# Kernel optimization log

Measured on AMD Instinct MI355X. Metric: run time of the kernel, lower is better.

Reference implementation:

```python
import jax, jax.numpy as jnp
import numpy as np

N, G, E = 100000, 32768, 1000000
F, H = 64, 64


def _mlp(x, w1, b1, w2, b2):
    # Linear -> SiLU -> Linear (matches nn.Sequential in the torch module)
    return jax.nn.silu(x @ w1 + b1) @ w2 + b2


def setup_inputs() -> dict:
    key = jax.random.key(0)
    ks = jax.random.split(key, 24)

    def lin(k, fan_in, fan_out):
        s = 1.0 / np.sqrt(fan_in)
        kw, kb = jax.random.split(k)
        w = jax.random.uniform(kw, (fan_in, fan_out), jnp.float32, -s, s)
        b = jax.random.uniform(kb, (fan_out,), jnp.float32, -s, s)
        return w, b

    node_w1, node_b1 = lin(ks[0], F, H)
    node_w2, node_b2 = lin(ks[1], H, H)
    edge_w1, edge_b1 = lin(ks[2], 6, H)
    edge_w2, edge_b2 = lin(ks[3], H, H)
    msg_w1, msg_b1 = lin(ks[4], 2 * H, H)
    msg_w2, msg_b2 = lin(ks[5], H, H)
    upd_w1, upd_b1 = lin(ks[6], H, H)
    upd_w2, upd_b2 = lin(ks[7], H, H)

    return {
        "node_features": jax.random.normal(ks[8], (N, F), jnp.float32),
        "node_pos": jax.random.normal(ks[9], (N, 3), jnp.float32),
        "grid_pos": jax.random.normal(ks[10], (G, 3), jnp.float32),
        "orientations": jax.random.normal(ks[11], (N, 3, 3), jnp.float32),
        "edge_index": jnp.stack([
            jax.random.randint(ks[12], (E,), 0, N),
            jax.random.randint(ks[13], (E,), 0, G),
        ]),
        "node_w1": node_w1, "node_b1": node_b1, "node_w2": node_w2, "node_b2": node_b2,
        "edge_w1": edge_w1, "edge_b1": edge_b1, "edge_w2": edge_w2, "edge_b2": edge_b2,
        "msg_w1": msg_w1, "msg_b1": msg_b1, "msg_w2": msg_w2, "msg_b2": msg_b2,
        "upd_w1": upd_w1, "upd_b1": upd_b1, "upd_w2": upd_w2, "upd_b2": upd_b2,
    }


def reference(node_features, node_pos, grid_pos, orientations, edge_index,
              node_w1, node_b1, node_w2, node_b2,
              edge_w1, edge_b1, edge_w2, edge_b2,
              msg_w1, msg_b1, msg_w2, msg_b2,
              upd_w1, upd_b1, upd_w2, upd_b2):
    source, target = edge_index[0], edge_index[1]
    num_grid = grid_pos.shape[0]

    # node MLP
    h_node = _mlp(node_features, node_w1, node_b1, node_w2, node_b2)  # [N,H]

    # per-edge message with orientation-aware projection
    pos_s = node_pos[source]                 # [E,3]
    rel = grid_pos[target] - pos_s           # [E,3]
    # bmm(rel[:,None,:], R[source]).squeeze(1) == einsum ei,eij->ej
    trel = jnp.einsum("ei,eij->ej", rel, orientations[source])
    edge_attr = jnp.concatenate([pos_s, trel], axis=-1)        # [E,6]
    e_feat = _mlp(edge_attr, edge_w1, edge_b1, edge_w2, edge_b2)
    msg_in = jnp.concatenate([h_node[source], e_feat], axis=-1)  # [E,2H]
    messages = _mlp(msg_in, msg_w1, msg_b1, msg_w2, msg_b2)      # [E,H]

    # scatter-mean into grid buckets (mask out-of-range targets)
    valid = (target >= 0) & (target < num_grid)
    idx = jnp.where(valid, target, 0)
    msg_masked = jnp.where(valid[:, None], messages, 0.0)
    sums = jax.ops.segment_sum(msg_masked, idx, num_segments=num_grid)
    cnts = jax.ops.segment_sum(valid.astype(jnp.float32), idx, num_segments=num_grid)
    grid_feat = sums / jnp.maximum(cnts, 1.0)[:, None]

    return _mlp(grid_feat, upd_w1, upd_b1, upd_w2, upd_b2)  # [G,H]
```

## Files before the change

### kernel.cpp

```cpp
#include <hip/hip_runtime.h>
#include <hip/hip_bf16.h>
#include <cstdint>

typedef __attribute__((ext_vector_type(8))) short short8;
typedef __attribute__((ext_vector_type(4))) float f32x4;
typedef unsigned short u16;

__device__ __forceinline__ float b2f(u16 u) {
  union { unsigned int i; float f; } v; v.i = ((unsigned int)u) << 16; return v.f;
}
__device__ __forceinline__ u16 f2b(float f) {
  __hip_bfloat16 h = __float2bfloat16(f);
  union { __hip_bfloat16 h; u16 u; } v; v.h = h; return v.u;
}
__device__ __forceinline__ float silu_f(float x) {
  return x * __builtin_amdgcn_rcpf(1.0f + __expf(-x));
}

__device__ __forceinline__ float loadF(const void* p, long i, int isf32) {
  if (isf32) return ((const float*)p)[i];
  return b2f(((const u16*)p)[i]);
}

__device__ __forceinline__ int sniffbit(u16 u) {
  unsigned e = (u >> 7) & 0xffu;
  return (e >= 0xC0u || (e < 0x40u && (u & 0x7fffu) != 0)) ? 1 : 0;
}

struct Ptrs { const void* p[20]; int n[20]; };

#define FW_EW1 0
#define FW_UW1 384
#define FW_UW2 4480
#define FW_UB1 8576
#define FW_UB2 8640
#define FW_EB1 8704
#define FW_EB2 8768
#define FW_MB1 8832
#define FW_MB2 8896
#define FW_TOTAL 8960

#define IMG_EW2 0
#define IMG_MW1 4608
#define IMG_MW2 13312
#define IMG_TOTAL 17920

#define PREP_BLOCKS 105
#define HIST_BLOCKS 1024

__global__ __launch_bounds__(256) void hist_detect_k(
    Ptrs a, const int* __restrict__ eidx, int* __restrict__ cnt8,
    int* __restrict__ flags, long E, int G)
{
  const int t = threadIdx.x;
  const int b = blockIdx.x;
  if (b < HIST_BLOCKS) {
    int* cs = cnt8 + (size_t)(b & 7) * G;
    long i = (long)b * 256 + t;
    const long stride = (long)HIST_BLOCKS * 256;
    for (; i < E; i += stride) {
      int tg = eidx[E + i];
      if (tg >= 0 && tg < G) atomicAdd(&cs[tg], 1);
    }
    return;
  }
  int j = b - HIST_BLOCKS;
  const u16* q = (const u16*)a.p[j];
  int n = a.n[j];
  int m = n < 4096 ? n : 4096;
  int cnt = 0;
  for (int i = t; i < m; i += 256) cnt += sniffbit(q[i]);
  __shared__ int tot;
  if (t == 0) tot = 0;
  __syncthreads();
  if (cnt) atomicAdd(&tot, cnt);
  __syncthreads();
  if (t == 0) flags[j] = (tot >= 2) ? 1 : 0;
}

__global__ __launch_bounds__(256) void scan_prep_node_k(
    Ptrs a, const int* __restrict__ flags,
    const int* __restrict__ cnt8, int* __restrict__ cursor8,
    int* __restrict__ bsum,
    u16* __restrict__ img, float* __restrict__ fw,
    u16* __restrict__ hout, int nrows, int G, int NB2)
{
  const int t = threadIdx.x;
  const int b = blockIdx.x;

  if (b < NB2) {
    __shared__ int sd[256];
    const long tot = 8L * G;
    long j0 = (long)b * 1024 + (long)t * 4;
    int v[4];
#pragma unroll
    for (int k = 0; k < 4; ++k) {
      long j = j0 + k;
      v[k] = (j < tot) ? cnt8[(size_t)(j & 7) * G + (j >> 3)] : 0;
    }
    int local = v[0] + v[1] + v[2] + v[3];
    sd[t] = local;
    __syncthreads();
    for (int off = 1; off < 256; off <<= 1) {
      int x2 = (t >= off) ? sd[t - off] : 0;
      __syncthreads();
      sd[t] += x2;
      __syncthreads();
    }
    int p = sd[t] - local;
#pragma unroll
    for (int k = 0; k < 4; ++k) {
      long j = j0 + k;
      if (j < tot) cursor8[(size_t)(j & 7) * G + (j >> 3)] = p;
      p += v[k];
    }
    if (t == 255) bsum[b] = sd[255];
    return;
  }

  if (b < NB2 + PREP_BLOCKS) {
    int i = (b - NB2) * 256 + t;
    if (i < IMG_TOTAL) {
      const void* bp; int fl; long si; bool real;
      if (i < IMG_MW1) { int nn = i / 72, k = i % 72; bp = a.p[10]; fl = flags[10]; real = k < 64; si = (long)k * 64 + nn; }
      else if (i < IMG_MW2) { int t2 = i - IMG_MW1; int nn = t2 / 136, k = t2 % 136; bp = a.p[12]; fl = flags[12]; real = k < 128; si = (long)k * 64 + nn; }
      else { int t2 = i - IMG_MW2; int nn = t2 / 72, k = t2 % 72; bp = a.p[14]; fl = flags[14]; real = k < 64; si = (long)k * 64 + nn; }
      u16 val = 0;
      if (real) val = f2b(loadF(bp, si, fl));
      img[i] = val;
    } else if (i < IMG_TOTAL + FW_TOTAL) {
      int j = i - IMG_TOTAL;
      const void* bp; int fl; long si;
      if (j < 384)        { bp = a.p[8];  fl = flags[8];  si = j; }
      else if (j < 4480)  { bp = a.p[16]; fl = flags[16]; si = j - 384; }
      else if (j < 8576)  { bp = a.p[18]; fl = flags[18]; si = j - 4480; }
      else {
        int bb = j - 8576; int seg = bb >> 6; si = bb & 63;
        switch (seg) {
          case 0: bp = a.p[17]; fl = flags[17]; break;
          case 1: bp = a.p[19]; fl = flags[19]; break;
          case 2: bp = a.p[9];  fl = flags[9];  break;
          case 3: bp = a.p[11]; fl = flags[11]; break;
          case 4: bp = a.p[13]; fl = flags[13]; break;
          default: bp = a.p[15]; fl = flags[15]; break;
        }
      }
      fw[j] = loadF(bp, si, fl);
    }
    return;
  }

  __shared__ float xs[64][68];
  __shared__ float w1s[64][68];
  __shared__ float w2s[64][68];
  __shared__ float b1s[64];
  __shared__ float b2s[64];
  const void* x = a.p[0];
  const int xf = flags[0], f1 = flags[4], fb1 = flags[5], f2 = flags[6], fb2 = flags[7];
  const long rbase = (long)(b - NB2 - PREP_BLOCKS) * 64;
  for (int i = t; i < 4096; i += 256) {
    int k = i >> 6, cc = i & 63;
    w1s[k][cc] = loadF(a.p[4], i, f1);
    w2s[k][cc] = loadF(a.p[6], i, f2);
  }
  if (t < 64) { b1s[t] = loadF(a.p[5], t, fb1); b2s[t] = loadF(a.p[7], t, fb2); }
  {
    int row = t >> 2, ch = t & 3;
    long rg = rbase + row;
    if (rg < nrows) {
      if (xf) {
        const float* xp = (const float*)x + rg * 64 + ch * 16;
#pragma unroll
        for (int m = 0; m < 16; ++m) xs[row][ch * 16 + m] = xp[m];
      } else {
        const u16* xp = (const u16*)x + rg * 64 + ch * 16;
#pragma unroll
        for (int m = 0; m < 16; ++m) xs[row][ch * 16 + m] = b2f(xp[m]);
      }
    } else {
#pragma unroll
      for (int m = 0; m < 16; ++m) xs[row][ch * 16 + m] = 0.f;
    }
  }
  __syncthreads();
  const int r0 = (t >> 4) * 4, c0 = (t & 15) * 4;
  float acc[4][4];
#pragma unroll
  for (int i = 0; i < 4; ++i)
#pragma unroll
    for (int j = 0; j < 4; ++j) acc[i][j] = b1s[c0 + j];
  for (int k = 0; k < 64; ++k) {
    float w0 = w1s[k][c0], w1v = w1s[k][c0 + 1], w2v = w1s[k][c0 + 2], w3v = w1s[k][c0 + 3];
#pragma unroll
    for (int i = 0; i < 4; ++i) {
      float av = xs[r0 + i][k];
      acc[i][0] = fmaf(av, w0, acc[i][0]);
      acc[i][1] = fmaf(av, w1v, acc[i][1]);
      acc[i][2] = fmaf(av, w2v, acc[i][2]);
      acc[i][3] = fmaf(av, w3v, acc[i][3]);
    }
  }
  __syncthreads();
#pragma unroll
  for (int i = 0; i < 4; ++i)
#pragma unroll
    for (int j = 0; j < 4; ++j) xs[r0 + i][c0 + j] = silu_f(acc[i][j]);
  __syncthreads();
  float acc2[4][4];
#pragma unroll
  for (int i = 0; i < 4; ++i)
#pragma unroll
    for (int j = 0; j < 4; ++j) acc2[i][j] = b2s[c0 + j];
  for (int k = 0; k < 64; ++k) {
    float w0 = w2s[k][c0], w1v = w2s[k][c0 + 1], w2v = w2s[k][c0 + 2], w3v = w2s[k][c0 + 3];
#pragma unroll
    for (int i = 0; i < 4; ++i) {
      float av = xs[r0 + i][k];
      acc2[i][0] = fmaf(av, w0, acc2[i][0]);
      acc2[i][1] = fmaf(av, w1v, acc2[i][1]);
      acc2[i][2] = fmaf(av, w2v, acc2[i][2]);
      acc2[i][3] = fmaf(av, w3v, acc2[i][3]);
    }
  }
#pragma unroll
  for (int i = 0; i < 4; ++i) {
    long rg = rbase + r0 + i;
    if (rg < nrows) {
#pragma unroll
      for (int j = 0; j < 4; ++j) hout[rg * 64 + c0 + j] = f2b(acc2[i][j]);
    }
  }
}

__global__ __launch_bounds__(256) void scat_k(const int* __restrict__ eidx,
                                              int* __restrict__ cursor8,
                                              const int* __restrict__ bsum,
                                              unsigned int* __restrict__ pkS,
                                              int* __restrict__ evp,
                                              long E, int G, int NB2) {
  __shared__ int bo[256];
  const int t = threadIdx.x;
  int v = (t < NB2) ? bsum[t] : 0;
  bo[t] = v;
  __syncthreads();
  for (int off = 1; off < 256; off <<= 1) {
    int x2 = (t >= off) ? bo[t - off] : 0;
    __syncthreads();
    bo[t] += x2;
    __syncthreads();
  }
  if (blockIdx.x == 0 && t == 0) *evp = bo[NB2 - 1];
  int excl = bo[t] - v;
  __syncthreads();
  bo[t] = excl;
  __syncthreads();
  const int c = blockIdx.x & 7;
  int* cur = cursor8 + (size_t)c * G;
  long i = (long)blockIdx.x * 256 + t;
  const long stride = (long)gridDim.x * 256;
  for (; i < E; i += stride) {
    int tg = eidx[E + i];
    if (tg >= 0 && tg < G) {
      int s = eidx[i];
      long j = ((long)tg << 3) | c;
      int p = atomicAdd(&cur[tg], 1) + bo[j >> 10];
      __builtin_nontemporal_store((unsigned int)s | ((unsigned int)tg << 17), pkS + p);
    }
  }
}

#define ETILES 4

__global__ __launch_bounds__(256, 4) void edge_kernel(
    const void* node_pos, const void* grid_pos, const void* orient,
    const unsigned int* __restrict__ pkS, const int* __restrict__ evp,
    const u16* __restrict__ h_node, const u16* __restrict__ img,
    const float* __restrict__ fw, const int* __restrict__ flags,
    float* __restrict__ sums, int G)
{
  __shared__ __align__(16) u16 pool[4][3328];
  __shared__ float w1e[6][64];
  __shared__ float biasE[4][64];

  const int t = threadIdx.x;
  const int pf = flags[1], gf = flags[2], of = flags[3];
  const int Ev = *evp;

  const int lane = t & 63, w = t >> 6;
  const int q = lane >> 4, c = lane & 15;
  const int m0 = w * 16;
  u16 (* __restrict__ ef1w)[72] = (u16 (*)[72])&pool[w][0];
  u16 (* __restrict__ hAw)[136] = (u16 (*)[136])&pool[w][1152];
  float (* __restrict__ msgfw)[66] = (float (*)[66])&pool[w][1152];
  const u16* wE2 = img + IMG_EW2;
  const u16* wM1 = img + IMG_MW1;
  const u16* wM2 = img + IMG_MW2;
  const f32x4 z = {0.f, 0.f, 0.f, 0.f};

  const long blockBase = (long)blockIdx.x * (ETILES * 64);

  unsigned int pkA = 0, pkB = 0, pkC = 0, pkD = 0;
  if (lane < 16) {
    long e0 = blockBase + m0 + lane;
    if (e0 < Ev)       pkA = pkS[e0];
    if (e0 + 64 < Ev)  pkB = pkS[e0 + 64];
    if (e0 + 128 < Ev) pkC = pkS[e0 + 128];
    if (e0 + 192 < Ev) pkD = pkS[e0 + 192];
  }

  float o0 = 0.f, o1 = 0.f, o2 = 0.f, o3 = 0.f, o4 = 0.f, o5 = 0.f,
        o6 = 0.f, o7 = 0.f, o8 = 0.f;
  float ps0 = 0.f, ps1 = 0.f, ps2 = 0.f, gp0 = 0.f, gp1 = 0.f, gp2 = 0.f;
  short8 hv0, hv1;
  int ptg, ntg;

  {
    int gs = (int)(pkA & 0x1FFFFu);
    int tgc = (int)(pkA >> 17);
    if (lane < 16) {
      ps0 = loadF(node_pos, (long)gs * 3 + 0, pf);
      ps1 = loadF(node_pos, (long)gs * 3 + 1, pf);
      ps2 = loadF(node_pos, (long)gs * 3 + 2, pf);
      gp0 = loadF(grid_pos, (long)tgc * 3 + 0, gf);
      gp1 = loadF(grid_pos, (long)tgc * 3 + 1, gf);
      gp2 = loadF(grid_pos, (long)tgc * 3 + 2, gf);
      o0 = loadF(orient, (long)gs * 9 + 0, of);
      o1 = loadF(orient, (long)gs * 9 + 1, of);
      o2 = loadF(orient, (long)gs * 9 + 2, of);
      o3 = loadF(orient, (long)gs * 9 + 3, of);
      o4 = loadF(orient, (long)gs * 9 + 4, of);
      o5 = loadF(orient, (long)gs * 9 + 5, of);
      o6 = loadF(orient, (long)gs * 9 + 6, of);
      o7 = loadF(orient, (long)gs * 9 + 7, of);
      o8 = loadF(orient, (long)gs * 9 + 8, of);
    }
    unsigned int pks = (unsigned int)__shfl((int)pkA, lane >> 2);
    int ss = (int)(pks & 0x1FFFFu);
    const u16* hp = h_node + (long)ss * 64 + (lane & 3) * 16;
    hv0 = *(const short8*)hp;
    hv1 = *(const short8*)(hp + 8);
    long gPrev = blockBase + m0 - 1;
    long gNext = blockBase + m0 + 16;
    ptg = (gPrev >= 0 && gPrev < Ev) ? (int)(pkS[gPrev] >> 17) : -2;
    ntg = (gNext < Ev) ? (int)(pkS[gNext] >> 17) : -2;
  }

  for (int i = t; i < 384; i += 256) w1e[i / 64][i % 64] = fw[FW_EW1 + i];
  { int seg = t >> 6, cc = t & 63; biasE[seg][cc] = fw[FW_EB1 + seg * 64 + cc]; }
  __syncthreads();

  for (int tile = 0; tile < ETILES; ++tile) {
    long base = blockBase + (long)tile * 64;
    if (base >= Ev) break;

    int mytg = -1;
    {
      long eg = base + m0 + lane;
      if (lane < 16) mytg = (eg < Ev) ? (int)(pkA >> 17) : -1;
      float rel0 = gp0 - ps0, rel1 = gp1 - ps1, rel2 = gp2 - ps2;
      float tr0 = rel0 * o0; tr0 = fmaf(rel1, o3, tr0); tr0 = fmaf(rel2, o6, tr0);
      float tr1 = rel0 * o1; tr1 = fmaf(rel1, o4, tr1); tr1 = fmaf(rel2, o7, tr1);
      float tr2 = rel0 * o2; tr2 = fmaf(rel1, o5, tr2); tr2 = fmaf(rel2, o8, tr2);
      int sl = lane >> 2;
      float a0 = __shfl(ps0, sl), a1 = __shfl(ps1, sl), a2 = __shfl(ps2, sl);
      float a3 = __shfl(tr0, sl), a4 = __shfl(tr1, sl), a5 = __shfl(tr2, sl);
      int er = lane >> 2, ch = lane & 3;
      *(short8*)&hAw[er][ch * 16] = hv0;
      *(short8*)&hAw[er][ch * 16 + 8] = hv1;
      int c0 = (lane & 3) * 16;
      __align__(16) u16 tmp[16];
#pragma unroll
      for (int j = 0; j < 16; ++j) {
        int cc = c0 + j;
        float acc = biasE[0][cc];
        acc = fmaf(a0, w1e[0][cc], acc);
        acc = fmaf(a1, w1e[1][cc], acc);
        acc = fmaf(a2, w1e[2][cc], acc);
        acc = fmaf(a3, w1e[3][cc], acc);
        acc = fmaf(a4, w1e[4][cc], acc);
        acc = fmaf(a5, w1e[5][cc], acc);
        tmp[j] = f2b(silu_f(acc));
      }
      *(short8*)&ef1w[er][c0] = *(const short8*)tmp;
      *(short8*)&ef1w[er][c0 + 8] = *(const short8*)(tmp + 8);
    }
    __builtin_amdgcn_wave_barrier();
    {
      short8 a0 = *(const short8*)&ef1w[c][q * 8];
      short8 a1 = *(const short8*)&ef1w[c][32 + q * 8];
#pragma unroll
      for (int nt = 0; nt < 4; ++nt) {
        short8 b0 = *(const short8*)&wE2[(nt * 16 + c) * 72 + q * 8];
        short8 b1v = *(const short8*)&wE2[(nt * 16 + c) * 72 + 32 + q * 8];
        f32x4 acc = __builtin_amdgcn_mfma_f32_16x16x32_bf16(a0, b0, z, 0, 0, 0);
        acc = __builtin_amdgcn_mfma_f32_16x16x32_bf16(a1, b1v, acc, 0, 0, 0);
#pragma unroll
        for (int r = 0; r < 4; ++r) {
          int row = q * 4 + r, col = nt * 16 + c;
          hAw[row][64 + col] = f2b(acc[r] + biasE[1][col]);
        }
      }
    }
    __builtin_amdgcn_wave_barrier();
    {
      short8 a0 = *(const short8*)&hAw[c][q * 8];
      short8 a1 = *(const short8*)&hAw[c][32 + q * 8];
      short8 a2 = *(const short8*)&hAw[c][64 + q * 8];
      short8 a3 = *(const short8*)&hAw[c][96 + q * 8];
#pragma unroll
      for (int nt = 0; nt < 4; ++nt) {
        const u16* wp = &wM1[(nt * 16 + c) * 136];
        f32x4 acc = __builtin_amdgcn_mfma_f32_16x16x32_bf16(a0, *(const short8*)(wp + q * 8), z, 0, 0, 0);
        acc = __builtin_amdgcn_mfma_f32_16x16x32_bf16(a1, *(const short8*)(wp + 32 + q * 8), acc, 0, 0, 0);
        acc = __builtin_amdgcn_mfma_f32_16x16x32_bf16(a2, *(const short8*)(wp + 64 + q * 8), acc, 0, 0, 0);
        acc = __builtin_amdgcn_mfma_f32_16x16x32_bf16(a3, *(const short8*)(wp + 96 + q * 8), acc, 0, 0, 0);
#pragma unroll
        for (int r = 0; r < 4; ++r) {
          int row = q * 4 + r, col = nt * 16 + c;
          ef1w[row][col] = f2b(silu_f(acc[r] + biasE[2][col]));
        }
      }
    }
    __builtin_amdgcn_wave_barrier();
    {
      short8 a0 = *(const short8*)&ef1w[c][q * 8];
      short8 a1 = *(const short8*)&ef1w[c][32 + q * 8];
      __builtin_amdgcn_wave_barrier();
#pragma unroll
      for (int nt = 0; nt < 4; ++nt) {
        short8 b0 = *(const short8*)&wM2[(nt * 16 + c) * 72 + q * 8];
        short8 b1v = *(const short8*)&wM2[(nt * 16 + c) * 72 + 32 + q * 8];
        f32x4 acc = __builtin_amdgcn_mfma_f32_16x16x32_bf16(a0, b0, z, 0, 0, 0);
        acc = __builtin_amdgcn_mfma_f32_16x16x32_bf16(a1, b1v, acc, 0, 0, 0);
#pragma unroll
        for (int r = 0; r < 4; ++r) {
          int row = q * 4 + r, col = nt * 16 + c;
          msgfw[row][col] = acc[r] + biasE[3][col];
        }
      }
    }
    __builtin_amdgcn_wave_barrier();

    __builtin_amdgcn_sched_barrier(0);
    if (tile + 1 < ETILES && base + 64 < Ev) {
      int gs2 = (int)(pkB & 0x1FFFFu);
      int tgc2 = (int)(pkB >> 17);
      if (lane < 16) {
        ps0 = loadF(node_pos, (long)gs2 * 3 + 0, pf);
        ps1 = loadF(node_pos, (long)gs2 * 3 + 1, pf);
        ps2 = loadF(node_pos, (long)gs2 * 3 + 2, pf);
        gp0 = loadF(grid_pos, (long)tgc2 * 3 + 0, gf);
        gp1 = loadF(grid_pos, (long)tgc2 * 3 + 1, gf);
        gp2 = loadF(grid_pos, (long)tgc2 * 3 + 2, gf);
        o0 = loadF(orient, (long)gs2 * 9 + 0, of);
        o1 = loadF(orient, (long)gs2 * 9 + 1, of);
        o2 = loadF(orient, (long)gs2 * 9 + 2, of);
        o3 = loadF(orient, (long)gs2 * 9 + 3, of);
        o4 = loadF(orient, (long)gs2 * 9 + 4, of);
        o5 = loadF(orient, (long)gs2 * 9 + 5, of);
        o6 = loadF(orient, (long)gs2 * 9 + 6, of);
        o7 = loadF(orient, (long)gs2 * 9 + 7, of);
        o8 = loadF(orient, (long)gs2 * 9 + 8, of);
      }
      unsigned int pks2 = (unsigned int)__shfl((int)pkB, lane >> 2);
      int ss2 = (int)(pks2 & 0x1FFFFu);
      const u16* hp2 = h_node + (long)ss2 * 64 + (lane & 3) * 16;
      hv0 = *(const short8*)hp2;
      hv1 = *(const short8*)(hp2 + 8);
    }
    __builtin_amdgcn_sched_barrier(0);

    {
      int col = lane;
      int cur = __shfl(mytg, 0);
      float run = msgfw[0][col];
      bool lopen = (ptg == cur);
#pragma unroll
      for (int r2 = 1; r2 < 16; ++r2) {
        int tg = __shfl(mytg, r2);
        float v = msgfw[r2][col];
        if (tg == cur) {
          run += v;
        } else {
          if (cur >= 0) {
            if (lopen) unsafeAtomicAdd(&sums[(long)cur * 64 + col], run);
            else sums[(long)cur * 64 + col] = run;
          }
          cur = tg; run = v; lopen = false;
        }
      }
      bool ropen = (ntg == cur);
      if (cur >= 0) {
        if (lopen || ropen) unsafeAtomicAdd(&sums[(long)cur * 64 + col], run);
        else sums[(long)cur * 64 + col] = run;
      }
    }
    __builtin_amdgcn_wave_barrier();

    if (tile + 1 < ETILES && base + 64 < Ev) {
      long gPrev = base + 64 + m0 - 1;
      long gNext = base + 64 + m0 + 16;
      ptg = (gPrev < Ev) ? (int)(pkS[gPrev] >> 17) : -2;
      ntg = (gNext < Ev) ? (int)(pkS[gNext] >> 17) : -2;
    }
    pkA = pkB; pkB = pkC; pkC = pkD;
  }
}

__global__ __launch_bounds__(256) void upd_mlp(
    const float* __restrict__ sums, const int* __restrict__ cnt8,
    const float* __restrict__ fw, float* __restrict__ out, int nrows)
{
  __shared__ float xs[64][68];
  __shared__ float w1s[64][68];
  __shared__ float w2s[64][68];
  __shared__ float b1s[64];
  __shared__ float b2s[64];
  const int t = threadIdx.x;
  const long rbase = (long)blockIdx.x * 64;
  for (int i = t; i < 4096; i += 256) {
    int k = i >> 6, cc = i & 63;
    w1s[k][cc] = fw[FW_UW1 + i];
    w2s[k][cc] = fw[FW_UW2 + i];
  }
  if (t < 64) { b1s[t] = fw[FW_UB1 + t]; b2s[t] = fw[FW_UB2 + t]; }
  {
    int row = t >> 2, ch = t & 3;
    long rg = rbase + row;
    if (rg < nrows) {
      int cn = 0;
#pragma unroll
      for (int cc = 0; cc < 8; ++cc) cn += cnt8[(size_t)cc * nrows + rg];
      float inv = 1.0f / fmaxf((float)cn, 1.0f);
      const float* p = sums + rg * 64 + ch * 16;
#pragma unroll
      for (int m = 0; m < 16; ++m) xs[row][ch * 16 + m] = p[m] * inv;
    } else {
#pragma unroll
      for (int m = 0; m < 16; ++m) xs[row][ch * 16 + m] = 0.f;
    }
  }
  __syncthreads();
  const int r0 = (t >> 4) * 4, c0 = (t & 15) * 4;
  float acc[4][4];
#pragma unroll
  for (int i = 0; i < 4; ++i)
#pragma unroll
    for (int j = 0; j < 4; ++j) acc[i][j] = b1s[c0 + j];
  for (int k = 0; k < 64; ++k) {
    float w0 = w1s[k][c0], w1v = w1s[k][c0 + 1], w2v = w1s[k][c0 + 2], w3v = w1s[k][c0 + 3];
#pragma unroll
    for (int i = 0; i < 4; ++i) {
      float av = xs[r0 + i][k];
      acc[i][0] = fmaf(av, w0, acc[i][0]);
      acc[i][1] = fmaf(av, w1v, acc[i][1]);
      acc[i][2] = fmaf(av, w2v, acc[i][2]);
      acc[i][3] = fmaf(av, w3v, acc[i][3]);
    }
  }
  __syncthreads();
#pragma unroll
  for (int i = 0; i < 4; ++i)
#pragma unroll
    for (int j = 0; j < 4; ++j) xs[r0 + i][c0 + j] = silu_f(acc[i][j]);
  __syncthreads();
  float acc2[4][4];
#pragma unroll
  for (int i = 0; i < 4; ++i)
#pragma unroll
    for (int j = 0; j < 4; ++j) acc2[i][j] = b2s[c0 + j];
  for (int k = 0; k < 64; ++k) {
    float w0 = w2s[k][c0], w1v = w2s[k][c0 + 1], w2v = w2s[k][c0 + 2], w3v = w2s[k][c0 + 3];
#pragma unroll
    for (int i = 0; i < 4; ++i) {
      float av = xs[r0 + i][k];
      acc2[i][0] = fmaf(av, w0, acc2[i][0]);
      acc2[i][1] = fmaf(av, w1v, acc2[i][1]);
      acc2[i][2] = fmaf(av, w2v, acc2[i][2]);
      acc2[i][3] = fmaf(av, w3v, acc2[i][3]);
    }
  }
#pragma unroll
  for (int i = 0; i < 4; ++i) {
    long rg = rbase + r0 + i;
    if (rg < nrows) {
#pragma unroll
      for (int j = 0; j < 4; ++j) out[rg * 64 + c0 + j] = acc2[i][j];
    }
  }
}

extern "C" void kernel_launch(void* const* d_in, const int* in_sizes, int n_in,
                              void* d_out, int out_size, void* d_ws, size_t ws_size,
                              hipStream_t stream) {
  const int N = in_sizes[1] / 3;
  const int G = in_sizes[2] / 3;
  const long E = (long)in_sizes[4] / 2;
  const int NB2 = (int)((8L * G + 1023) / 1024);
  const int nodeBlocks = (N + 63) / 64;

  char* ws = (char*)d_ws;
  float* sums = (float*)ws;
  size_t off = (size_t)G * 256;
  int* cnt8 = (int*)(ws + off);     off += (size_t)G * 32;
  int* cursor8 = (int*)(ws + off);  off += (size_t)G * 32;
  int* bsum = (int*)(ws + off);     off += 1024;
  int* evp = (int*)(ws + off);      off += 256;
  int* flags = (int*)(ws + off);    off += 256;
  unsigned int* pkS = (unsigned int*)(ws + off); off += (size_t)E * 4;
  u16* h_node = (u16*)(ws + off);   off += (size_t)N * 128;
  u16* img = (u16*)(ws + off);      off += (size_t)IMG_TOTAL * 2;
  float* fw = (float*)(ws + off);

  hipMemsetAsync(ws, 0, (size_t)G * 288, stream);

  Ptrs a;
  const int map[20] = {0,1,2,3, 5,6,7,8, 9,10,11,12, 13,14,15,16, 17,18,19,20};
  for (int i = 0; i < 20; ++i) { a.p[i] = d_in[map[i]]; a.n[i] = in_sizes[map[i]]; }

  hist_detect_k<<<HIST_BLOCKS + 20, 256, 0, stream>>>(
      a, (const int*)d_in[4], cnt8, flags, E, G);
  scan_prep_node_k<<<NB2 + PREP_BLOCKS + nodeBlocks, 256, 0, stream>>>(
      a, flags, cnt8, cursor8, bsum, img, fw, h_node, N, G, NB2);
  scat_k<<<1024, 256, 0, stream>>>((const int*)d_in[4], cursor8, bsum, pkS, evp, E, G, NB2);
  edge_kernel<<<(int)((E + ETILES * 64 - 1) / (ETILES * 64)), 256, 0, stream>>>(
      d_in[1], d_in[2], d_in[3], pkS, evp, h_node, img, fw, flags, sums, G);
  upd_mlp<<<(G + 63) / 64, 256, 0, stream>>>(sums, cnt8, fw, (float*)d_out, G);
}
```

Before: 446.1 us.

## Feed gathered node features and first edge layer directly as MFMA A-fragments

Each lane now gathers h_node and computes the first edge-MLP layer in the exact 16x16x32 MFMA A-operand layout (row c, k-slice q*8 and 32+q*8). This removes the LDS round-trip for the concatenated message input and for the first edge hidden layer, along with one wave barrier. The per-wave LDS pool shrinks to match. In exchange, each lane evaluates 16 first-layer columns spread across two ranges, and the global h_node loads become two 16-byte pieces 64 bytes apart instead of 32 contiguous bytes.

```diff
diff --git a/kernel.cpp b/kernel.cpp
--- a/kernel.cpp
+++ b/kernel.cpp
@@ -278,7 +278,7 @@
     const float* __restrict__ fw, const int* __restrict__ flags,
     float* __restrict__ sums, int G)
 {
-  __shared__ __align__(16) u16 pool[4][3328];
+  __shared__ __align__(16) u16 pool[4][2304];
   __shared__ float w1e[6][64];
   __shared__ float biasE[4][64];
 
@@ -289,9 +289,9 @@
   const int lane = t & 63, w = t >> 6;
   const int q = lane >> 4, c = lane & 15;
   const int m0 = w * 16;
-  u16 (* __restrict__ ef1w)[72] = (u16 (*)[72])&pool[w][0];
-  u16 (* __restrict__ hAw)[136] = (u16 (*)[136])&pool[w][1152];
-  float (* __restrict__ msgfw)[66] = (float (*)[66])&pool[w][1152];
+  u16 (* __restrict__ efeat)[72] = (u16 (*)[72])&pool[w][0];
+  u16 (* __restrict__ ef1w)[72]  = (u16 (*)[72])&pool[w][1152];
+  float (* __restrict__ msgfw)[66] = (float (*)[66])&pool[w][0];
   const u16* wE2 = img + IMG_EW2;
   const u16* wM1 = img + IMG_MW1;
   const u16* wM2 = img + IMG_MW2;
@@ -334,11 +334,11 @@
       o7 = loadF(orient, (long)gs * 9 + 7, of);
       o8 = loadF(orient, (long)gs * 9 + 8, of);
     }
-    unsigned int pks = (unsigned int)__shfl((int)pkA, lane >> 2);
+    unsigned int pks = (unsigned int)__shfl((int)pkA, c);
     int ss = (int)(pks & 0x1FFFFu);
-    const u16* hp = h_node + (long)ss * 64 + (lane & 3) * 16;
+    const u16* hp = h_node + (long)ss * 64 + q * 8;
     hv0 = *(const short8*)hp;
-    hv1 = *(const short8*)(hp + 8);
+    hv1 = *(const short8*)(hp + 32);
     long gPrev = blockBase + m0 - 1;
     long gNext = blockBase + m0 + 16;
     ptg = (gPrev >= 0 && gPrev < Ev) ? (int)(pkS[gPrev] >> 17) : -2;
@@ -354,6 +354,7 @@
     if (base >= Ev) break;
 
     int mytg = -1;
+    short8 a0e, a1e;
     {
       long eg = base + m0 + lane;
       if (lane < 16) mytg = (eg < Ev) ? (int)(pkA >> 17) : -1;
@@ -361,57 +362,56 @@
       float tr0 = rel0 * o0; tr0 = fmaf(rel1, o3, tr0); tr0 = fmaf(rel2, o6, tr0);
       float tr1 = rel0 * o1; tr1 = fmaf(rel1, o4, tr1); tr1 = fmaf(rel2, o7, tr1);
       float tr2 = rel0 * o2; tr2 = fmaf(rel1, o5, tr2); tr2 = fmaf(rel2, o8, tr2);
-      int sl = lane >> 2;
-      float a0 = __shfl(ps0, sl), a1 = __shfl(ps1, sl), a2 = __shfl(ps2, sl);
-      float a3 = __shfl(tr0, sl), a4 = __shfl(tr1, sl), a5 = __shfl(tr2, sl);
-      int er = lane >> 2, ch = lane & 3;
-      *(short8*)&hAw[er][ch * 16] = hv0;
-      *(short8*)&hAw[er][ch * 16 + 8] = hv1;
-      int c0 = (lane & 3) * 16;
-      __align__(16) u16 tmp[16];
-#pragma unroll
-      for (int j = 0; j < 16; ++j) {
-        int cc = c0 + j;
-        float acc = biasE[0][cc];
-        acc = fmaf(a0, w1e[0][cc], acc);
-        acc = fmaf(a1, w1e[1][cc], acc);
-        acc = fmaf(a2, w1e[2][cc], acc);
-        acc = fmaf(a3, w1e[3][cc], acc);
-        acc = fmaf(a4, w1e[4][cc], acc);
-        acc = fmaf(a5, w1e[5][cc], acc);
-        tmp[j] = f2b(silu_f(acc));
-      }
-      *(short8*)&ef1w[er][c0] = *(const short8*)tmp;
-      *(short8*)&ef1w[er][c0 + 8] = *(const short8*)(tmp + 8);
-    }
-    __builtin_amdgcn_wave_barrier();
+      float a0 = __shfl(ps0, c), a1 = __shfl(ps1, c), a2 = __shfl(ps2, c);
+      float a3 = __shfl(tr0, c), a4 = __shfl(tr1, c), a5 = __shfl(tr2, c);
+      __align__(16) u16 tA[8], tB[8];
+#pragma unroll
+      for (int jj = 0; jj < 8; ++jj) {
+        int colA = q * 8 + jj;
+        int colB = 32 + q * 8 + jj;
+        float accA = biasE[0][colA];
+        accA = fmaf(a0, w1e[0][colA], accA);
+        accA = fmaf(a1, w1e[1][colA], accA);
+        accA = fmaf(a2, w1e[2][colA], accA);
+        accA = fmaf(a3, w1e[3][colA], accA);
+        accA = fmaf(a4, w1e[4][colA], accA);
+        accA = fmaf(a5, w1e[5][colA], accA);
+        tA[jj] = f2b(silu_f(accA));
+        float accB = biasE[0][colB];
+        accB = fmaf(a0, w1e[0][colB], accB);
+        accB = fmaf(a1, w1e[1][colB], accB);
+        accB = fmaf(a2, w1e[2][colB], accB);
+        accB = fmaf(a3, w1e[3][colB], accB);
+        accB = fmaf(a4, w1e[4][colB], accB);
+        accB = fmaf(a5, w1e[5][colB], accB);
+        tB[jj] = f2b(silu_f(accB));
+      }
+      a0e = *(const short8*)tA;
+      a1e = *(const short8*)tB;
+    }
     {
-      short8 a0 = *(const short8*)&ef1w[c][q * 8];
-      short8 a1 = *(const short8*)&ef1w[c][32 + q * 8];
 #pragma unroll
       for (int nt = 0; nt < 4; ++nt) {
         short8 b0 = *(const short8*)&wE2[(nt * 16 + c) * 72 + q * 8];
         short8 b1v = *(const short8*)&wE2[(nt * 16 + c) * 72 + 32 + q * 8];
-        f32x4 acc = __builtin_amdgcn_mfma_f32_16x16x32_bf16(a0, b0, z, 0, 0, 0);
-        acc = __builtin_amdgcn_mfma_f32_16x16x32_bf16(a1, b1v, acc, 0, 0, 0);
+        f32x4 acc = __builtin_amdgcn_mfma_f32_16x16x32_bf16(a0e, b0, z, 0, 0, 0);
+        acc = __builtin_amdgcn_mfma_f32_16x16x32_bf16(a1e, b1v, acc, 0, 0, 0);
 #pragma unroll
         for (int r = 0; r < 4; ++r) {
           int row = q * 4 + r, col = nt * 16 + c;
-          hAw[row][64 + col] = f2b(acc[r] + biasE[1][col]);
+          efeat[row][col] = f2b(acc[r] + biasE[1][col]);
         }
       }
     }
     __builtin_amdgcn_wave_barrier();
     {
-      short8 a0 = *(const short8*)&hAw[c][q * 8];
-      short8 a1 = *(const short8*)&hAw[c][32 + q * 8];
-      short8 a2 = *(const short8*)&hAw[c][64 + q * 8];
-      short8 a3 = *(const short8*)&hAw[c][96 + q * 8];
+      short8 a2 = *(const short8*)&efeat[c][q * 8];
+      short8 a3 = *(const short8*)&efeat[c][32 + q * 8];
 #pragma unroll
       for (int nt = 0; nt < 4; ++nt) {
         const u16* wp = &wM1[(nt * 16 + c) * 136];
-        f32x4 acc = __builtin_amdgcn_mfma_f32_16x16x32_bf16(a0, *(const short8*)(wp + q * 8), z, 0, 0, 0);
-        acc = __builtin_amdgcn_mfma_f32_16x16x32_bf16(a1, *(const short8*)(wp + 32 + q * 8), acc, 0, 0, 0);
+        f32x4 acc = __builtin_amdgcn_mfma_f32_16x16x32_bf16(hv0, *(const short8*)(wp + q * 8), z, 0, 0, 0);
+        acc = __builtin_amdgcn_mfma_f32_16x16x32_bf16(hv1, *(const short8*)(wp + 32 + q * 8), acc, 0, 0, 0);
         acc = __builtin_amdgcn_mfma_f32_16x16x32_bf16(a2, *(const short8*)(wp + 64 + q * 8), acc, 0, 0, 0);
         acc = __builtin_amdgcn_mfma_f32_16x16x32_bf16(a3, *(const short8*)(wp + 96 + q * 8), acc, 0, 0, 0);
 #pragma unroll
@@ -462,11 +462,11 @@
         o7 = loadF(orient, (long)gs2 * 9 + 7, of);
         o8 = loadF(orient, (long)gs2 * 9 + 8, of);
       }
-      unsigned int pks2 = (unsigned int)__shfl((int)pkB, lane >> 2);
+      unsigned int pks2 = (unsigned int)__shfl((int)pkB, c);
       int ss2 = (int)(pks2 & 0x1FFFFu);
-      const u16* hp2 = h_node + (long)ss2 * 64 + (lane & 3) * 16;
+      const u16* hp2 = h_node + (long)ss2 * 64 + q * 8;
       hv0 = *(const short8*)hp2;
-      hv1 = *(const short8*)(hp2 + 8);
+      hv1 = *(const short8*)(hp2 + 32);
     }
     __builtin_amdgcn_sched_barrier(0);
 
```

Result: slower. 464.0 us (+4.0%).

## Regroup kernels: fuse histogram with node MLP, split scan, multi-tile MLP blocks

Applied to the files above, without the earlier changes.

Moves the target histogram out of the dtype-detect kernel and into the same launch as weight prep and the node MLP, so the atomics overlap with MLP compute. The prefix scan becomes its own kernel. The node and update MLP blocks now each process four 64-row tiles, so the shared-memory weight load is amortised over more rows. Fewer blocks means less parallelism for the MLPs, and there is one extra kernel launch.

```diff
diff --git a/kernel.cpp b/kernel.cpp
--- a/kernel.cpp
+++ b/kernel.cpp
@@ -47,24 +47,12 @@
 
 #define PREP_BLOCKS 105
 #define HIST_BLOCKS 1024
-
-__global__ __launch_bounds__(256) void hist_detect_k(
-    Ptrs a, const int* __restrict__ eidx, int* __restrict__ cnt8,
-    int* __restrict__ flags, long E, int G)
+#define MLP_TILES 4
+
+__global__ __launch_bounds__(256) void detect_k(Ptrs a, int* __restrict__ flags)
 {
   const int t = threadIdx.x;
-  const int b = blockIdx.x;
-  if (b < HIST_BLOCKS) {
-    int* cs = cnt8 + (size_t)(b & 7) * G;
-    long i = (long)b * 256 + t;
-    const long stride = (long)HIST_BLOCKS * 256;
-    for (; i < E; i += stride) {
-      int tg = eidx[E + i];
-      if (tg >= 0 && tg < G) atomicAdd(&cs[tg], 1);
-    }
-    return;
-  }
-  int j = b - HIST_BLOCKS;
+  const int j = blockIdx.x;
   const u16* q = (const u16*)a.p[j];
   int n = a.n[j];
   int m = n < 4096 ? n : 4096;
@@ -78,48 +66,28 @@
   if (t == 0) flags[j] = (tot >= 2) ? 1 : 0;
 }
 
-__global__ __launch_bounds__(256) void scan_prep_node_k(
-    Ptrs a, const int* __restrict__ flags,
-    const int* __restrict__ cnt8, int* __restrict__ cursor8,
-    int* __restrict__ bsum,
+__global__ __launch_bounds__(256) void fused_hist_prep_node_k(
+    Ptrs a, const int* __restrict__ eidx, int* __restrict__ cnt8,
+    const int* __restrict__ flags,
     u16* __restrict__ img, float* __restrict__ fw,
-    u16* __restrict__ hout, int nrows, int G, int NB2)
+    u16* __restrict__ hout, int nrows, int G, long E)
 {
   const int t = threadIdx.x;
   const int b = blockIdx.x;
 
-  if (b < NB2) {
-    __shared__ int sd[256];
-    const long tot = 8L * G;
-    long j0 = (long)b * 1024 + (long)t * 4;
-    int v[4];
-#pragma unroll
-    for (int k = 0; k < 4; ++k) {
-      long j = j0 + k;
-      v[k] = (j < tot) ? cnt8[(size_t)(j & 7) * G + (j >> 3)] : 0;
-    }
-    int local = v[0] + v[1] + v[2] + v[3];
-    sd[t] = local;
-    __syncthreads();
-    for (int off = 1; off < 256; off <<= 1) {
-      int x2 = (t >= off) ? sd[t - off] : 0;
-      __syncthreads();
-      sd[t] += x2;
-      __syncthreads();
-    }
-    int p = sd[t] - local;
-#pragma unroll
-    for (int k = 0; k < 4; ++k) {
-      long j = j0 + k;
-      if (j < tot) cursor8[(size_t)(j & 7) * G + (j >> 3)] = p;
-      p += v[k];
-    }
-    if (t == 255) bsum[b] = sd[255];
+  if (b < HIST_BLOCKS) {
+    int* cs = cnt8 + (size_t)(b & 7) * G;
+    long i = (long)b * 256 + t;
+    const long stride = (long)HIST_BLOCKS * 256;
+    for (; i < E; i += stride) {
+      int tg = eidx[E + i];
+      if (tg >= 0 && tg < G) atomicAdd(&cs[tg], 1);
+    }
     return;
   }
 
-  if (b < NB2 + PREP_BLOCKS) {
-    int i = (b - NB2) * 256 + t;
+  if (b < HIST_BLOCKS + PREP_BLOCKS) {
+    int i = (b - HIST_BLOCKS) * 256 + t;
     if (i < IMG_TOTAL) {
       const void* bp; int fl; long si; bool real;
       if (i < IMG_MW1) { int nn = i / 72, k = i % 72; bp = a.p[10]; fl = flags[10]; real = k < 64; si = (long)k * 64 + nn; }
@@ -157,79 +125,119 @@
   __shared__ float b2s[64];
   const void* x = a.p[0];
   const int xf = flags[0], f1 = flags[4], fb1 = flags[5], f2 = flags[6], fb2 = flags[7];
-  const long rbase = (long)(b - NB2 - PREP_BLOCKS) * 64;
+  const long obase = (long)(b - HIST_BLOCKS - PREP_BLOCKS) * (64 * MLP_TILES);
   for (int i = t; i < 4096; i += 256) {
     int k = i >> 6, cc = i & 63;
     w1s[k][cc] = loadF(a.p[4], i, f1);
     w2s[k][cc] = loadF(a.p[6], i, f2);
   }
   if (t < 64) { b1s[t] = loadF(a.p[5], t, fb1); b2s[t] = loadF(a.p[7], t, fb2); }
-  {
-    int row = t >> 2, ch = t & 3;
-    long rg = rbase + row;
-    if (rg < nrows) {
-      if (xf) {
-        const float* xp = (const float*)x + rg * 64 + ch * 16;
-#pragma unroll
-        for (int m = 0; m < 16; ++m) xs[row][ch * 16 + m] = xp[m];
+  const int r0 = (t >> 4) * 4, c0 = (t & 15) * 4;
+
+  for (int tt = 0; tt < MLP_TILES; ++tt) {
+    const long rbase = obase + (long)tt * 64;
+    if (rbase >= nrows) break;
+    {
+      int row = t >> 2, ch = t & 3;
+      long rg = rbase + row;
+      if (rg < nrows) {
+        if (xf) {
+          const float* xp = (const float*)x + rg * 64 + ch * 16;
+#pragma unroll
+          for (int m = 0; m < 16; ++m) xs[row][ch * 16 + m] = xp[m];
+        } else {
+          const u16* xp = (const u16*)x + rg * 64 + ch * 16;
+#pragma unroll
+          for (int m = 0; m < 16; ++m) xs[row][ch * 16 + m] = b2f(xp[m]);
+        }
       } else {
-        const u16* xp = (const u16*)x + rg * 64 + ch * 16;
-#pragma unroll
-        for (int m = 0; m < 16; ++m) xs[row][ch * 16 + m] = b2f(xp[m]);
-      }
-    } else {
-#pragma unroll
-      for (int m = 0; m < 16; ++m) xs[row][ch * 16 + m] = 0.f;
-    }
-  }
+#pragma unroll
+        for (int m = 0; m < 16; ++m) xs[row][ch * 16 + m] = 0.f;
+      }
+    }
+    __syncthreads();
+    float acc[4][4];
+#pragma unroll
+    for (int i = 0; i < 4; ++i)
+#pragma unroll
+      for (int j = 0; j < 4; ++j) acc[i][j] = b1s[c0 + j];
+    for (int k = 0; k < 64; ++k) {
+      float w0 = w1s[k][c0], w1v = w1s[k][c0 + 1], w2v = w1s[k][c0 + 2], w3v = w1s[k][c0 + 3];
+#pragma unroll
+      for (int i = 0; i < 4; ++i) {
+        float av = xs[r0 + i][k];
+        acc[i][0] = fmaf(av, w0, acc[i][0]);
+        acc[i][1] = fmaf(av, w1v, acc[i][1]);
+        acc[i][2] = fmaf(av, w2v, acc[i][2]);
+        acc[i][3] = fmaf(av, w3v, acc[i][3]);
+      }
+    }
+    __syncthreads();
+#pragma unroll
+    for (int i = 0; i < 4; ++i)
+#pragma unroll
+      for (int j = 0; j < 4; ++j) xs[r0 + i][c0 + j] = silu_f(acc[i][j]);
+    __syncthreads();
+    float acc2[4][4];
+#pragma unroll
+    for (int i = 0; i < 4; ++i)
+#pragma unroll
+      for (int j = 0; j < 4; ++j) acc2[i][j] = b2s[c0 + j];
+    for (int k = 0; k < 64; ++k) {
+      float w0 = w2s[k][c0], w1v = w2s[k][c0 + 1], w2v = w2s[k][c0 + 2], w3v = w2s[k][c0 + 3];
+#pragma unroll
+      for (int i = 0; i < 4; ++i) {
+        float av = xs[r0 + i][k];
+        acc2[i][0] = fmaf(av, w0, acc2[i][0]);
+        acc2[i][1] = fmaf(av, w1v, acc2[i][1]);
+        acc2[i][2] = fmaf(av, w2v, acc2[i][2]);
+        acc2[i][3] = fmaf(av, w3v, acc2[i][3]);
+      }
+    }
+#pragma unroll
+    for (int i = 0; i < 4; ++i) {
+      long rg = rbase + r0 + i;
+      if (rg < nrows) {
+#pragma unroll
+        for (int j = 0; j < 4; ++j) hout[rg * 64 + c0 + j] = f2b(acc2[i][j]);
+      }
+    }
+    __syncthreads();
+  }
+}
+
+__global__ __launch_bounds__(256) void scan_k(
+    const int* __restrict__ cnt8, int* __restrict__ cursor8,
+    int* __restrict__ bsum, int G)
+{
+  const int t = threadIdx.x;
+  const int b = blockIdx.x;
+  __shared__ int sd[256];
+  const long tot = 8L * G;
+  long j0 = (long)b * 1024 + (long)t * 4;
+  int v[4];
+#pragma unroll
+  for (int k = 0; k < 4; ++k) {
+    long j = j0 + k;
+    v[k] = (j < tot) ? cnt8[(size_t)(j & 7) * G + (j >> 3)] : 0;
+  }
+  int local = v[0] + v[1] + v[2] + v[3];
+  sd[t] = local;
   __syncthreads();
-  const int r0 = (t >> 4) * 4, c0 = (t & 15) * 4;
-  float acc[4][4];
-#pragma unroll
-  for (int i = 0; i < 4; ++i)
-#pragma unroll
-    for (int j = 0; j < 4; ++j) acc[i][j] = b1s[c0 + j];
-  for (int k = 0; k < 64; ++k) {
-    float w0 = w1s[k][c0], w1v = w1s[k][c0 + 1], w2v = w1s[k][c0 + 2], w3v = w1s[k][c0 + 3];
-#pragma unroll
-    for (int i = 0; i < 4; ++i) {
-      float av = xs[r0 + i][k];
-      acc[i][0] = fmaf(av, w0, acc[i][0]);
-      acc[i][1] = fmaf(av, w1v, acc[i][1]);
-      acc[i][2] = fmaf(av, w2v, acc[i][2]);
-      acc[i][3] = fmaf(av, w3v, acc[i][3]);
-    }
-  }
-  __syncthreads();
-#pragma unroll
-  for (int i = 0; i < 4; ++i)
-#pragma unroll
-    for (int j = 0; j < 4; ++j) xs[r0 + i][c0 + j] = silu_f(acc[i][j]);
-  __syncthreads();
-  float acc2[4][4];
-#pragma unroll
-  for (int i = 0; i < 4; ++i)
-#pragma unroll
-    for (int j = 0; j < 4; ++j) acc2[i][j] = b2s[c0 + j];
-  for (int k = 0; k < 64; ++k) {
-    float w0 = w2s[k][c0], w1v = w2s[k][c0 + 1], w2v = w2s[k][c0 + 2], w3v = w2s[k][c0 + 3];
-#pragma unroll
-    for (int i = 0; i < 4; ++i) {
-      float av = xs[r0 + i][k];
-      acc2[i][0] = fmaf(av, w0, acc2[i][0]);
-      acc2[i][1] = fmaf(av, w1v, acc2[i][1]);
-      acc2[i][2] = fmaf(av, w2v, acc2[i][2]);
-      acc2[i][3] = fmaf(av, w3v, acc2[i][3]);
-    }
-  }
-#pragma unroll
-  for (int i = 0; i < 4; ++i) {
-    long rg = rbase + r0 + i;
-    if (rg < nrows) {
-#pragma unroll
-      for (int j = 0; j < 4; ++j) hout[rg * 64 + c0 + j] = f2b(acc2[i][j]);
-    }
-  }
+  for (int off = 1; off < 256; off <<= 1) {
+    int x2 = (t >= off) ? sd[t - off] : 0;
+    __syncthreads();
+    sd[t] += x2;
+    __syncthreads();
+  }
+  int p = sd[t] - local;
+#pragma unroll
+  for (int k = 0; k < 4; ++k) {
+    long j = j0 + k;
+    if (j < tot) cursor8[(size_t)(j & 7) * G + (j >> 3)] = p;
+    p += v[k];
+  }
+  if (t == 255) bsum[b] = sd[255];
 }
 
 __global__ __launch_bounds__(256) void scat_k(const int* __restrict__ eidx,
@@ -517,76 +525,82 @@
   __shared__ float b1s[64];
   __shared__ float b2s[64];
   const int t = threadIdx.x;
-  const long rbase = (long)blockIdx.x * 64;
+  const long obase = (long)blockIdx.x * (64 * MLP_TILES);
   for (int i = t; i < 4096; i += 256) {
     int k = i >> 6, cc = i & 63;
     w1s[k][cc] = fw[FW_UW1 + i];
     w2s[k][cc] = fw[FW_UW2 + i];
   }
   if (t < 64) { b1s[t] = fw[FW_UB1 + t]; b2s[t] = fw[FW_UB2 + t]; }
-  {
-    int row = t >> 2, ch = t & 3;
-    long rg = rbase + row;
-    if (rg < nrows) {
-      int cn = 0;
-#pragma unroll
-      for (int cc = 0; cc < 8; ++cc) cn += cnt8[(size_t)cc * nrows + rg];
-      float inv = 1.0f / fmaxf((float)cn, 1.0f);
-      const float* p = sums + rg * 64 + ch * 16;
-#pragma unroll
-      for (int m = 0; m < 16; ++m) xs[row][ch * 16 + m] = p[m] * inv;
-    } else {
-#pragma unroll
-      for (int m = 0; m < 16; ++m) xs[row][ch * 16 + m] = 0.f;
-    }
-  }
-  __syncthreads();
   const int r0 = (t >> 4) * 4, c0 = (t & 15) * 4;
-  float acc[4][4];
-#pragma unroll
-  for (int i = 0; i < 4; ++i)
-#pragma unroll
-    for (int j = 0; j < 4; ++j) acc[i][j] = b1s[c0 + j];
-  for (int k = 0; k < 64; ++k) {
-    float w0 = w1s[k][c0], w1v = w1s[k][c0 + 1], w2v = w1s[k][c0 + 2], w3v = w1s[k][c0 + 3];
+
+  for (int tt = 0; tt < MLP_TILES; ++tt) {
+    const long rbase = obase + (long)tt * 64;
+    if (rbase >= nrows) break;
+    {
+      int row = t >> 2, ch = t & 3;
+      long rg = rbase + row;
+      if (rg < nrows) {
+        int cn = 0;
+#pragma unroll
+        for (int cc = 0; cc < 8; ++cc) cn += cnt8[(size_t)cc * nrows + rg];
+        float inv = 1.0f / fmaxf((float)cn, 1.0f);
+        const float* p = sums + rg * 64 + ch * 16;
+#pragma unroll
+        for (int m = 0; m < 16; ++m) xs[row][ch * 16 + m] = p[m] * inv;
+      } else {
+#pragma unroll
+        for (int m = 0; m < 16; ++m) xs[row][ch * 16 + m] = 0.f;
+      }
+    }
+    __syncthreads();
+    float acc[4][4];
+#pragma unroll
+    for (int i = 0; i < 4; ++i)
+#pragma unroll
+      for (int j = 0; j < 4; ++j) acc[i][j] = b1s[c0 + j];
+    for (int k = 0; k < 64; ++k) {
+      float w0 = w1s[k][c0], w1v = w1s[k][c0 + 1], w2v = w1s[k][c0 + 2], w3v = w1s[k][c0 + 3];
+#pragma unroll
+      for (int i = 0; i < 4; ++i) {
+        float av = xs[r0 + i][k];
+        acc[i][0] = fmaf(av, w0, acc[i][0]);
+        acc[i][1] = fmaf(av, w1v, acc[i][1]);
+        acc[i][2] = fmaf(av, w2v, acc[i][2]);
+        acc[i][3] = fmaf(av, w3v, acc[i][3]);
+      }
+    }
+    __syncthreads();
+#pragma unroll
+    for (int i = 0; i < 4; ++i)
+#pragma unroll
+      for (int j = 0; j < 4; ++j) xs[r0 + i][c0 + j] = silu_f(acc[i][j]);
+    __syncthreads();
+    float acc2[4][4];
+#pragma unroll
+    for (int i = 0; i < 4; ++i)
+#pragma unroll
+      for (int j = 0; j < 4; ++j) acc2[i][j] = b2s[c0 + j];
+    for (int k = 0; k < 64; ++k) {
+      float w0 = w2s[k][c0], w1v = w2s[k][c0 + 1], w2v = w2s[k][c0 + 2], w3v = w2s[k][c0 + 3];
+#pragma unroll
+      for (int i = 0; i < 4; ++i) {
+        float av = xs[r0 + i][k];
+        acc2[i][0] = fmaf(av, w0, acc2[i][0]);
+        acc2[i][1] = fmaf(av, w1v, acc2[i][1]);
+        acc2[i][2] = fmaf(av, w2v, acc2[i][2]);
+        acc2[i][3] = fmaf(av, w3v, acc2[i][3]);
+      }
+    }
 #pragma unroll
     for (int i = 0; i < 4; ++i) {
-      float av = xs[r0 + i][k];
-      acc[i][0] = fmaf(av, w0, acc[i][0]);
-      acc[i][1] = fmaf(av, w1v, acc[i][1]);
-      acc[i][2] = fmaf(av, w2v, acc[i][2]);
-      acc[i][3] = fmaf(av, w3v, acc[i][3]);
-    }
-  }
-  __syncthreads();
-#pragma unroll
-  for (int i = 0; i < 4; ++i)
-#pragma unroll
-    for (int j = 0; j < 4; ++j) xs[r0 + i][c0 + j] = silu_f(acc[i][j]);
-  __syncthreads();
-  float acc2[4][4];
-#pragma unroll
-  for (int i = 0; i < 4; ++i)
-#pragma unroll
-    for (int j = 0; j < 4; ++j) acc2[i][j] = b2s[c0 + j];
-  for (int k = 0; k < 64; ++k) {
-    float w0 = w2s[k][c0], w1v = w2s[k][c0 + 1], w2v = w2s[k][c0 + 2], w3v = w2s[k][c0 + 3];
-#pragma unroll
-    for (int i = 0; i < 4; ++i) {
-      float av = xs[r0 + i][k];
-      acc2[i][0] = fmaf(av, w0, acc2[i][0]);
-      acc2[i][1] = fmaf(av, w1v, acc2[i][1]);
-      acc2[i][2] = fmaf(av, w2v, acc2[i][2]);
-      acc2[i][3] = fmaf(av, w3v, acc2[i][3]);
-    }
-  }
-#pragma unroll
-  for (int i = 0; i < 4; ++i) {
-    long rg = rbase + r0 + i;
-    if (rg < nrows) {
-#pragma unroll
-      for (int j = 0; j < 4; ++j) out[rg * 64 + c0 + j] = acc2[i][j];
-    }
+      long rg = rbase + r0 + i;
+      if (rg < nrows) {
+#pragma unroll
+        for (int j = 0; j < 4; ++j) out[rg * 64 + c0 + j] = acc2[i][j];
+      }
+    }
+    __syncthreads();
   }
 }
 
@@ -597,7 +611,8 @@
   const int G = in_sizes[2] / 3;
   const long E = (long)in_sizes[4] / 2;
   const int NB2 = (int)((8L * G + 1023) / 1024);
-  const int nodeBlocks = (N + 63) / 64;
+  const int nodeOuter = (N + 64 * MLP_TILES - 1) / (64 * MLP_TILES);
+  const int updOuter = (G + 64 * MLP_TILES - 1) / (64 * MLP_TILES);
 
   char* ws = (char*)d_ws;
   float* sums = (float*)ws;
@@ -618,12 +633,12 @@
   const int map[20] = {0,1,2,3, 5,6,7,8, 9,10,11,12, 13,14,15,16, 17,18,19,20};
   for (int i = 0; i < 20; ++i) { a.p[i] = d_in[map[i]]; a.n[i] = in_sizes[map[i]]; }
 
-  hist_detect_k<<<HIST_BLOCKS + 20, 256, 0, stream>>>(
-      a, (const int*)d_in[4], cnt8, flags, E, G);
-  scan_prep_node_k<<<NB2 + PREP_BLOCKS + nodeBlocks, 256, 0, stream>>>(
-      a, flags, cnt8, cursor8, bsum, img, fw, h_node, N, G, NB2);
+  detect_k<<<20, 256, 0, stream>>>(a, flags);
+  fused_hist_prep_node_k<<<HIST_BLOCKS + PREP_BLOCKS + nodeOuter, 256, 0, stream>>>(
+      a, (const int*)d_in[4], cnt8, flags, img, fw, h_node, N, G, E);
+  scan_k<<<NB2, 256, 0, stream>>>(cnt8, cursor8, bsum, G);
   scat_k<<<1024, 256, 0, stream>>>((const int*)d_in[4], cursor8, bsum, pkS, evp, E, G, NB2);
   edge_kernel<<<(int)((E + ETILES * 64 - 1) / (ETILES * 64)), 256, 0, stream>>>(
       d_in[1], d_in[2], d_in[3], pkS, evp, h_node, img, fw, flags, sums, G);
-  upd_mlp<<<(G + 63) / 64, 256, 0, stream>>>(sums, cnt8, fw, (float*)d_out, G);
-}
+  upd_mlp<<<updOuter, 256, 0, stream>>>(sums, cnt8, fw, (float*)d_out, G);
+}
```

Result: slower. 470.8 us (+5.5%).
